# Kernel optimization log

Hardware: AMD Instinct MI355X
Metric: run time of the kernel (lower is better)

The kernel has to match this reference:

```python
import jax, jax.numpy as jnp
import numpy as np

B, D = 2048, 1024
TEMP = 0.1
LAMBDA_CS_REG = 0.5


def setup_inputs() -> dict:
    key = jax.random.key(0)
    k1, k2, k3, k4, k5 = jax.random.split(key, 5)
    return {
        "english": jax.random.normal(k1, (B, D), dtype=jnp.float32),
        "etok": jax.random.normal(k2, (B, D), dtype=jnp.float32),
        "ktoe": jax.random.normal(k3, (B, D), dtype=jnp.float32),
        "korean": jax.random.normal(k4, (B, D), dtype=jnp.float32),
        "cs_ratios": jax.random.uniform(k5, (B,), dtype=jnp.float32),
    }


def _l2norm(x):
    return x / jnp.linalg.norm(x, axis=1, keepdims=True)


def reference(english, etok, ktoe, korean, cs_ratios):
    e = _l2norm(english)   # [B,D]
    et = _l2norm(etok)
    kt = _l2norm(ktoe)
    k = _l2norm(korean)
    bsz = e.shape[0]

    # Stack the 4 embedding types: order [english, korean, etok, ktoe]
    embs = jnp.stack([e, k, et, kt])           # [4,B,D]

    # Similarities of each anchor row i against every row j of every type t.
    S_e = jnp.einsum("bd,tnd->tbn", e, embs) / TEMP   # [4,B,B] english anchors
    S_k = jnp.einsum("bd,tnd->tbn", k, embs) / TEMP   # [4,B,B] korean anchors
    exp_Se = jnp.exp(S_e)
    exp_Sk = jnp.exp(S_k)

    diag_e = jnp.diagonal(exp_Se, axis1=1, axis2=2)   # [4,B] exp(sim(anchor_i, type_i))
    diag_k = jnp.diagonal(exp_Sk, axis1=1, axis2=2)

    # Negatives: all 4 types for every j != i.
    neg_e = exp_Se.sum(axis=(0, 2)) - diag_e.sum(axis=0)   # [B]
    neg_k = exp_Sk.sum(axis=(0, 2)) - diag_k.sum(axis=0)

    # Positives: eng anchor -> {etok_i, ktoe_i, korean_i}; kor anchor -> {etok_i, ktoe_i, english_i}
    num_e = diag_e[1] + diag_e[2] + diag_e[3]
    num_k = diag_k[0] + diag_k[2] + diag_k[3]

    loss_e = -jnp.log(num_e / (num_e + neg_e))
    loss_k = -jnp.log(num_k / (num_k + neg_k))
    contrastive_loss = (loss_e + loss_k).sum() / (2 * bsz)

    # Code-switch regularization
    r = cs_ratios[:, None]                              # [B,1]
    etok_reg = jnp.linalg.norm(et - (r * e + (1 - r) * k), axis=1)
    ktoe_reg = jnp.linalg.norm(kt - ((1 - r) * e + r * k), axis=1)
    cs_reg_loss = (etok_reg + ktoe_reg).sum() / bsz

    total_loss = contrastive_loss + LAMBDA_CS_REG * cs_reg_loss
    return total_loss, contrastive_loss, cs_reg_loss
```

## Files before the change

### kernel.cpp

```cpp
#include <hip/hip_runtime.h>
#include <math.h>

#define NB   2048
#define ND   1024
#define INV_TEMP 10.0f
#define LAMBDA_CS 0.5f

using short8  = __attribute__((ext_vector_type(8))) short;
using floatx4 = __attribute__((ext_vector_type(4))) float;

__device__ __forceinline__ ushort f32_to_bf16_rne(float f) {
  union { float f; unsigned u; } v; v.f = f;
  unsigned u = v.u;
  u += 0x7FFFu + ((u >> 16) & 1u);
  return (ushort)(u >> 16);
}

__global__ __launch_bounds__(256) void k_norm_reg(
    const float* __restrict__ e, const float* __restrict__ k,
    const float* __restrict__ et, const float* __restrict__ kt,
    const float* __restrict__ ratios,
    ushort* __restrict__ M, float* __restrict__ reg_partial)
{
  const int b = blockIdx.x, tid = threadIdx.x;
  const int wave = tid >> 6, lane = tid & 63;

  float4 ve  = ((const float4*)(e  + (size_t)b * ND))[tid];
  float4 vk  = ((const float4*)(k  + (size_t)b * ND))[tid];
  float4 vet = ((const float4*)(et + (size_t)b * ND))[tid];
  float4 vkt = ((const float4*)(kt + (size_t)b * ND))[tid];

  float s0 = ve.x*ve.x + ve.y*ve.y + ve.z*ve.z + ve.w*ve.w;
  float s1 = vk.x*vk.x + vk.y*vk.y + vk.z*vk.z + vk.w*vk.w;
  float s2 = vet.x*vet.x + vet.y*vet.y + vet.z*vet.z + vet.w*vet.w;
  float s3 = vkt.x*vkt.x + vkt.y*vkt.y + vkt.z*vkt.z + vkt.w*vkt.w;
  #pragma unroll
  for (int o = 1; o < 64; o <<= 1) {
    s0 += __shfl_xor(s0, o); s1 += __shfl_xor(s1, o);
    s2 += __shfl_xor(s2, o); s3 += __shfl_xor(s3, o);
  }
  __shared__ float red[4][4];
  if (lane == 0) { red[wave][0] = s0; red[wave][1] = s1; red[wave][2] = s2; red[wave][3] = s3; }
  __syncthreads();
  const float ie  = 1.0f / sqrtf(red[0][0] + red[1][0] + red[2][0] + red[3][0]);
  const float ik  = 1.0f / sqrtf(red[0][1] + red[1][1] + red[2][1] + red[3][1]);
  const float iet = 1.0f / sqrtf(red[0][2] + red[1][2] + red[2][2] + red[3][2]);
  const float ikt = 1.0f / sqrtf(red[0][3] + red[1][3] + red[2][3] + red[3][3]);

  {
    ushort o4[4];
    o4[0] = f32_to_bf16_rne(ve.x * ie);  o4[1] = f32_to_bf16_rne(ve.y * ie);
    o4[2] = f32_to_bf16_rne(ve.z * ie);  o4[3] = f32_to_bf16_rne(ve.w * ie);
    *(ushort4*)(M + ((size_t)0 * NB + b) * ND + tid * 4) = *(ushort4*)o4;
    o4[0] = f32_to_bf16_rne(vk.x * ik);  o4[1] = f32_to_bf16_rne(vk.y * ik);
    o4[2] = f32_to_bf16_rne(vk.z * ik);  o4[3] = f32_to_bf16_rne(vk.w * ik);
    *(ushort4*)(M + ((size_t)1 * NB + b) * ND + tid * 4) = *(ushort4*)o4;
    o4[0] = f32_to_bf16_rne(vet.x * iet); o4[1] = f32_to_bf16_rne(vet.y * iet);
    o4[2] = f32_to_bf16_rne(vet.z * iet); o4[3] = f32_to_bf16_rne(vet.w * iet);
    *(ushort4*)(M + ((size_t)2 * NB + b) * ND + tid * 4) = *(ushort4*)o4;
    o4[0] = f32_to_bf16_rne(vkt.x * ikt); o4[1] = f32_to_bf16_rne(vkt.y * ikt);
    o4[2] = f32_to_bf16_rne(vkt.z * ikt); o4[3] = f32_to_bf16_rne(vkt.w * ikt);
    *(ushort4*)(M + ((size_t)3 * NB + b) * ND + tid * 4) = *(ushort4*)o4;
  }

  const float r = ratios[b], rm = 1.0f - r;
  float a1 = 0.f, a2 = 0.f;
  {
    float en, kn, d1, d2;
    en = ve.x*ie; kn = vk.x*ik;
    d1 = vet.x*iet - (r*en + rm*kn); d2 = vkt.x*ikt - (rm*en + r*kn);
    a1 += d1*d1; a2 += d2*d2;
    en = ve.y*ie; kn = vk.y*ik;
    d1 = vet.y*iet - (r*en + rm*kn); d2 = vkt.y*ikt - (rm*en + r*kn);
    a1 += d1*d1; a2 += d2*d2;
    en = ve.z*ie; kn = vk.z*ik;
    d1 = vet.z*iet - (r*en + rm*kn); d2 = vkt.z*ikt - (rm*en + r*kn);
    a1 += d1*d1; a2 += d2*d2;
    en = ve.w*ie; kn = vk.w*ik;
    d1 = vet.w*iet - (r*en + rm*kn); d2 = vkt.w*ikt - (rm*en + r*kn);
    a1 += d1*d1; a2 += d2*d2;
  }
  #pragma unroll
  for (int o = 1; o < 64; o <<= 1) { a1 += __shfl_xor(a1, o); a2 += __shfl_xor(a2, o); }
  __shared__ float red2[4][2];
  if (lane == 0) { red2[wave][0] = a1; red2[wave][1] = a2; }
  __syncthreads();
  if (tid == 0) {
    float t1 = red2[0][0] + red2[1][0] + red2[2][0] + red2[3][0];
    float t2 = red2[0][1] + red2[1][1] + red2[2][1] + red2[3][1];
    reg_partial[b] = sqrtf(t1) + sqrtf(t2);
  }
}


#define STAGE_A(TT, HH, BUF) do {                                              \
  _Pragma("unroll")                                                            \
  for (int L_ = 0; L_ < 2; ++L_) {                                             \
    const int u_ = L_ * 512 + tid;                                             \
    const int rr_ = u_ >> 3;                                                   \
    const int sc_ = ((u_ & 7) * 16) ^ ((rr_ & 7) << 4);                        \
    const ushort* gp_ = M + (size_t)(i0 + (HH)*128 + rr_) * ND + (TT)*64 + (sc_ >> 1); \
    __builtin_amdgcn_global_load_lds(                                          \
        (const __attribute__((address_space(1))) unsigned int*)gp_,            \
        (__attribute__((address_space(3))) unsigned int*)&As[BUF][(HH)*8192 + L_*4096 + wave*512], \
        16, 0, 0);                                                             \
  }                                                                            \
} while (0)

#define STAGE_B(TT, HH, BUF) do {                                              \
  _Pragma("unroll")                                                            \
  for (int L_ = 0; L_ < 2; ++L_) {                                             \
    const int u_ = L_ * 512 + tid;                                             \
    const int rr_ = u_ >> 3;                                                   \
    const int sc_ = ((u_ & 7) * 16) ^ ((rr_ & 7) << 4);                        \
    const ushort* gp_ = M + (size_t)(j0 + (HH)*128 + rr_) * ND + (TT)*64 + (sc_ >> 1); \
    __builtin_amdgcn_global_load_lds(                                          \
        (const __attribute__((address_space(1))) unsigned int*)gp_,            \
        (__attribute__((address_space(3))) unsigned int*)&Bs[BUF][(HH)*8192 + L_*4096 + wave*512], \
        16, 0, 0);                                                             \
  }                                                                            \
} while (0)

#define PHASE(BUF, MQ, KK, LOADB, WAIT, STMT) do {                             \
  short8 af_[4];                                                               \
  _Pragma("unroll")                                                            \
  for (int mi_ = 0; mi_ < 4; ++mi_) {                                          \
    const int row_ = wrow + ((MQ)*4 + mi_)*16 + m;                             \
    const int cb_ = ((KK)*64 + q*16) ^ ((row_ & 7) << 4);                      \
    af_[mi_] = *(const short8*)&As[BUF][row_*64 + (cb_ >> 1)];                 \
  }                                                                            \
  if (LOADB) {                                                                 \
    _Pragma("unroll")                                                          \
    for (int ni_ = 0; ni_ < 4; ++ni_) {                                        \
      const int rb_ = wcol + ni_*16 + m;                                       \
      const int cb_ = ((KK)*64 + q*16) ^ ((rb_ & 7) << 4);                     \
      bfr[KK][ni_] = *(const short8*)&Bs[BUF][rb_*64 + (cb_ >> 1)];            \
    }                                                                          \
  }                                                                            \
  STMT;                                                                        \
  __builtin_amdgcn_s_barrier();                                                \
  asm volatile("s_waitcnt lgkmcnt(0)" ::: "memory");                           \
  __builtin_amdgcn_s_setprio(1);                                               \
  _Pragma("unroll")                                                            \
  for (int mi_ = 0; mi_ < 4; ++mi_)                                            \
    _Pragma("unroll")                                                          \
    for (int ni_ = 0; ni_ < 4; ++ni_)                                          \
      acc[(MQ)*4 + mi_][ni_] = __builtin_amdgcn_mfma_f32_16x16x32_bf16(        \
          af_[mi_], bfr[KK][ni_], acc[(MQ)*4 + mi_][ni_], 0, 0, 0);            \
  __builtin_amdgcn_s_setprio(0);                                               \
  if (WAIT) asm volatile("s_waitcnt vmcnt(4)" ::: "memory");                   \
  __builtin_amdgcn_s_barrier();                                                \
} while (0)

__global__ __launch_bounds__(512, 2) void k_gemm_exp_rowsum(
    const ushort* __restrict__ M,
    float* __restrict__ rsp,
    float* __restrict__ diag)
{
  __shared__ __align__(16) ushort As[2][16384];
  __shared__ __align__(16) ushort Bs[2][16384];

  int bx, by;
  {
    int idx = blockIdx.x;
    if (idx < 256) { by = idx >> 4; bx = 16 + (idx & 15); }
    else {
      int t = idx - 256; by = 0;
      while (t >= 16 - by) { t -= 16 - by; ++by; }
      bx = by + t;
    }
  }
  const bool sym = (bx < 16) && (bx > by);
  const int i0 = by * 256;
  const int j0 = bx * 256;

  const int tid  = threadIdx.x;
  const int wave = tid >> 6;
  const int lane = tid & 63;
  const int q = lane >> 4;
  const int m = lane & 15;
  const int wr = wave >> 2;
  const int wc = wave & 3;
  const int wrow = wr * 128;
  const int wcol = wc * 64;

  floatx4 acc[8][4] = {};
  short8 bfr[2][4];

  STAGE_A(0, 0, 0); STAGE_A(0, 1, 0);
  STAGE_B(0, 0, 0); STAGE_B(0, 1, 0);
  STAGE_B(1, 0, 1); STAGE_B(1, 1, 1);
  asm volatile("s_waitcnt vmcnt(4)" ::: "memory");
  __builtin_amdgcn_s_barrier();

  #pragma unroll 1
  for (int i = 0; i < 8; ++i) {
    const int t1 = 2*i + 1;
    const int t2 = (2*i + 2) & 15;
    const int t3 = (2*i + 3) & 15;
    PHASE(0, 0, 0, 1, 0, STAGE_A(t1, 0, 1));
    PHASE(0, 0, 1, 1, 0, STAGE_A(t1, 1, 1));
    PHASE(0, 1, 0, 0, 0, STAGE_B(t2, 0, 0));
    PHASE(0, 1, 1, 0, 1, STAGE_B(t2, 1, 0));
    PHASE(1, 0, 0, 1, 0, STAGE_A(t2, 0, 0));
    PHASE(1, 0, 1, 1, 0, STAGE_A(t2, 1, 0));
    PHASE(1, 1, 0, 0, 0, STAGE_B(t3, 0, 1));
    PHASE(1, 1, 1, 0, 1, STAGE_B(t3, 1, 1));
  }

  __syncthreads();

  float* redR = (float*)&As[0][0];
  float* redC = redR + 1024;

  float colAcc[4] = {0.f, 0.f, 0.f, 0.f};
  #pragma unroll
  for (int mi = 0; mi < 8; ++mi) {
    #pragma unroll
    for (int r = 0; r < 4; ++r) {
      const int ig = i0 + wrow + mi * 16 + q * 4 + r;
      float s = 0.f;
      #pragma unroll
      for (int ni = 0; ni < 4; ++ni) {
        const float v = __expf(acc[mi][ni][r] * INV_TEMP);
        s += v;
        colAcc[ni] += v;
        const int jg = j0 + wcol + ni * 16 + m;
        if (((ig ^ jg) & (NB - 1)) == 0) {
          diag[(((ig >> 11) << 2) + (jg >> 11)) * NB + (ig & (NB - 1))] = v;
        }
      }
      s += __shfl_xor(s, 1);
      s += __shfl_xor(s, 2);
      s += __shfl_xor(s, 4);
      s += __shfl_xor(s, 8);
      if (m == 0) redR[wc * 256 + wrow + mi * 16 + q * 4 + r] = s;
    }
  }
  #pragma unroll
  for (int ni = 0; ni < 4; ++ni) {
    float c = colAcc[ni];
    c += __shfl_xor(c, 16);
    c += __shfl_xor(c, 32);
    if (q == 0) redC[wr * 256 + wcol + ni * 16 + m] = c;
  }
  __syncthreads();
  if (tid < 256) {
    const float rs = redR[tid] + redR[256 + tid] + redR[512 + tid] + redR[768 + tid];
    rsp[(size_t)bx * 4096 + i0 + tid] = rs;
    if (sym) {
      const float cs = redC[tid] + redC[256 + tid];
      rsp[(size_t)by * 4096 + j0 + tid] = cs;
    }
  }
}

__global__ __launch_bounds__(1024) void k_final(
    const float* __restrict__ rsp, const float* __restrict__ diag,
    const float* __restrict__ reg_partial, float* __restrict__ out)
{
  const int tid = threadIdx.x;
  const int wave = tid >> 6, lane = tid & 63;
  float l = 0.f, g = 0.f;
  #pragma unroll
  for (int h = 0; h < 2; ++h) {
    const int n = tid + h * 1024;
    float se = 0.f, sk = 0.f;
    #pragma unroll 8
    for (int s = 0; s < 32; ++s) {
      se += rsp[s * 4096 + n];
      sk += rsp[s * 4096 + 2048 + n];
    }
    const float d_ee  = diag[0 * NB + n];
    const float d_ek  = diag[1 * NB + n];
    const float d_eet = diag[2 * NB + n];
    const float d_ekt = diag[3 * NB + n];
    const float d_kk  = diag[5 * NB + n];
    const float d_ket = diag[6 * NB + n];
    const float d_kkt = diag[7 * NB + n];
    const float num_e = d_ek + d_eet + d_ekt;
    const float num_k = d_ek + d_ket + d_kkt;
    l += logf((se - d_ee) / num_e) + logf((sk - d_kk) / num_k);
    g += reg_partial[n];
  }
  #pragma unroll
  for (int o = 1; o < 64; o <<= 1) { l += __shfl_xor(l, o); g += __shfl_xor(g, o); }
  __shared__ float rl[16], rg[16];
  if (lane == 0) { rl[wave] = l; rg[wave] = g; }
  __syncthreads();
  if (tid == 0) {
    float L = 0.f, G = 0.f;
    #pragma unroll
    for (int i = 0; i < 16; ++i) { L += rl[i]; G += rg[i]; }
    const float contrastive = L * (1.0f / (2.0f * NB));
    const float cs = G * (1.0f / NB);
    out[0] = contrastive + LAMBDA_CS * cs;
    out[1] = contrastive;
    out[2] = cs;
  }
}

extern "C" void kernel_launch(void* const* d_in, const int* in_sizes, int n_in,
                              void* d_out, int out_size, void* d_ws, size_t ws_size,
                              hipStream_t stream) {
  const float* english = (const float*)d_in[0];
  const float* etok    = (const float*)d_in[1];
  const float* ktoe    = (const float*)d_in[2];
  const float* korean  = (const float*)d_in[3];
  const float* ratios  = (const float*)d_in[4];

  char* ws = (char*)d_ws;
  const size_t OFF_M    = 0;
  const size_t OFF_RSP  = OFF_M + (size_t)8192 * 1024 * 2;
  const size_t OFF_DIAG = OFF_RSP + (size_t)32 * 4096 * 4;
  const size_t OFF_REG  = OFF_DIAG + 8 * NB * sizeof(float);

  ushort* M           = (ushort*)(ws + OFF_M);
  float* rsp          = (float*)(ws + OFF_RSP);
  float* diag         = (float*)(ws + OFF_DIAG);
  float* reg_partial  = (float*)(ws + OFF_REG);

  k_norm_reg<<<dim3(NB), 256, 0, stream>>>(english, korean, etok, ktoe, ratios, M, reg_partial);
  k_gemm_exp_rowsum<<<dim3(392), 512, 0, stream>>>(M, rsp, diag);
  k_final<<<dim3(1), 1024, 0, stream>>>(rsp, diag, reg_partial, (float*)d_out);
}
```

Baseline: 171.9 us.

## Accumulate row sums atomically, remap GEMM block order, issue staging loads earlier

New measurement: 169.7 us. Within noise of the previous version (-1.3%).

```diff
diff --git a/kernel.cpp b/kernel.cpp
--- a/kernel.cpp
+++ b/kernel.cpp
@@ -20,7 +20,8 @@
     const float* __restrict__ e, const float* __restrict__ k,
     const float* __restrict__ et, const float* __restrict__ kt,
     const float* __restrict__ ratios,
-    ushort* __restrict__ M, float* __restrict__ reg_partial)
+    ushort* __restrict__ M, float* __restrict__ reg_partial,
+    float* __restrict__ rowsum)
 {
   const int b = blockIdx.x, tid = threadIdx.x;
   const int wave = tid >> 6, lane = tid & 63;
@@ -89,6 +90,8 @@
     float t1 = red2[0][0] + red2[1][0] + red2[2][0] + red2[3][0];
     float t2 = red2[0][1] + red2[1][1] + red2[2][1] + red2[3][1];
     reg_partial[b] = sqrtf(t1) + sqrtf(t2);
+    rowsum[b] = 0.f;
+    rowsum[NB + b] = 0.f;
   }
 }
 
@@ -122,6 +125,7 @@
 } while (0)
 
 #define PHASE(BUF, MQ, KK, LOADB, WAIT, STMT) do {                             \
+  STMT;                                                                        \
   short8 af_[4];                                                               \
   _Pragma("unroll")                                                            \
   for (int mi_ = 0; mi_ < 4; ++mi_) {                                          \
@@ -137,7 +141,6 @@
       bfr[KK][ni_] = *(const short8*)&Bs[BUF][rb_*64 + (cb_ >> 1)];            \
     }                                                                          \
   }                                                                            \
-  STMT;                                                                        \
   __builtin_amdgcn_s_barrier();                                                \
   asm volatile("s_waitcnt lgkmcnt(0)" ::: "memory");                           \
   __builtin_amdgcn_s_setprio(1);                                               \
@@ -154,7 +157,7 @@
 
 __global__ __launch_bounds__(512, 2) void k_gemm_exp_rowsum(
     const ushort* __restrict__ M,
-    float* __restrict__ rsp,
+    float* __restrict__ rowsum,
     float* __restrict__ diag)
 {
   __shared__ __align__(16) ushort As[2][16384];
@@ -162,7 +165,7 @@
 
   int bx, by;
   {
-    int idx = blockIdx.x;
+    int idx = (blockIdx.x & 7) * 49 + (blockIdx.x >> 3);
     if (idx < 256) { by = idx >> 4; bx = 16 + (idx & 15); }
     else {
       int t = idx - 256; by = 0;
@@ -247,16 +250,16 @@
   __syncthreads();
   if (tid < 256) {
     const float rs = redR[tid] + redR[256 + tid] + redR[512 + tid] + redR[768 + tid];
-    rsp[(size_t)bx * 4096 + i0 + tid] = rs;
+    atomicAdd(&rowsum[i0 + tid], rs);
     if (sym) {
       const float cs = redC[tid] + redC[256 + tid];
-      rsp[(size_t)by * 4096 + j0 + tid] = cs;
+      atomicAdd(&rowsum[j0 + tid], cs);
     }
   }
 }
 
 __global__ __launch_bounds__(1024) void k_final(
-    const float* __restrict__ rsp, const float* __restrict__ diag,
+    const float* __restrict__ rowsum, const float* __restrict__ diag,
     const float* __restrict__ reg_partial, float* __restrict__ out)
 {
   const int tid = threadIdx.x;
@@ -265,12 +268,8 @@
   #pragma unroll
   for (int h = 0; h < 2; ++h) {
     const int n = tid + h * 1024;
-    float se = 0.f, sk = 0.f;
-    #pragma unroll 8
-    for (int s = 0; s < 32; ++s) {
-      se += rsp[s * 4096 + n];
-      sk += rsp[s * 4096 + 2048 + n];
-    }
+    const float se = rowsum[n];
+    const float sk = rowsum[NB + n];
     const float d_ee  = diag[0 * NB + n];
     const float d_ek  = diag[1 * NB + n];
     const float d_eet = diag[2 * NB + n];
@@ -311,16 +310,16 @@
 
   char* ws = (char*)d_ws;
   const size_t OFF_M    = 0;
-  const size_t OFF_RSP  = OFF_M + (size_t)8192 * 1024 * 2;
-  const size_t OFF_DIAG = OFF_RSP + (size_t)32 * 4096 * 4;
+  const size_t OFF_ROW  = OFF_M + (size_t)8192 * 1024 * 2;
+  const size_t OFF_DIAG = OFF_ROW + (size_t)4096 * 4;
   const size_t OFF_REG  = OFF_DIAG + 8 * NB * sizeof(float);
 
   ushort* M           = (ushort*)(ws + OFF_M);
-  float* rsp          = (float*)(ws + OFF_RSP);
+  float* rowsum       = (float*)(ws + OFF_ROW);
   float* diag         = (float*)(ws + OFF_DIAG);
   float* reg_partial  = (float*)(ws + OFF_REG);
 
-  k_norm_reg<<<dim3(NB), 256, 0, stream>>>(english, korean, etok, ktoe, ratios, M, reg_partial);
-  k_gemm_exp_rowsum<<<dim3(392), 512, 0, stream>>>(M, rsp, diag);
-  k_final<<<dim3(1), 1024, 0, stream>>>(rsp, diag, reg_partial, (float*)d_out);
-}
+  k_norm_reg<<<dim3(NB), 256, 0, stream>>>(english, korean, etok, ktoe, ratios, M, reg_partial, rowsum);
+  k_gemm_exp_rowsum<<<dim3(392), 512, 0, stream>>>(M, rowsum, diag);
+  k_final<<<dim3(1), 1024, 0, stream>>>(rowsum, diag, reg_partial, (float*)d_out);
+}
```
